# Kernel optimization log

Measured on AMD Instinct MI355X. Metric: run time of the kernel, lower is better.

## Reference

```python
import jax, jax.numpy as jnp
import numpy as np

NEG = -1e30  # finite stand-in for -inf so softmax grads stay clean


def setup_inputs() -> dict:
    key = jax.random.key(0)
    k1, k2 = jax.random.split(key)
    C, D = 8192, 512
    gt_class_embeddings = jax.random.normal(k1, (C, D), dtype=jnp.float32)
    w = jax.random.normal(k2, (C, D), dtype=jnp.float32)
    return {"gt_class_embeddings": gt_class_embeddings, "w": w}


def reference(gt_class_embeddings, w):
    # L2-normalize class embeddings, cosine-similarity matrix S (diag == 1)
    G = gt_class_embeddings / jnp.linalg.norm(gt_class_embeddings, axis=-1, keepdims=True)
    S = G @ G.T  # [C, C]
    C = S.shape[0]
    off_diag = ~jnp.eye(C, dtype=bool)

    # seSoftmax: per-row softmax over entries != 1 (off-diagonal); diagonal stays 1
    P = jax.nn.softmax(jnp.where(off_diag, S, NEG), axis=-1)
    S2 = jnp.where(off_diag, P, 1.0)

    # argsort(-S2)[1] == most similar (diag value 1 always ranks first),
    # argsort(-S2)[-1] == least similar == row min (softmax values < 1)
    ms = jnp.argmax(jnp.where(off_diag, S2, NEG), axis=-1)  # [C]
    ls = jnp.argmin(jnp.where(off_diag, S2, -NEG), axis=-1)  # [C]

    rows = jnp.arange(C)
    margin = S2[rows, ms] - S2[rows, ls]  # [C]

    d_ms = jnp.sqrt(jnp.sum((w - w[ms]) ** 2, axis=-1))  # [C]
    d_ls = jnp.sqrt(jnp.sum((w - w[ls]) ** 2, axis=-1))  # [C]

    loss = jnp.mean(jnp.maximum(0.0, d_ms - d_ls + margin))
    return loss
```

## Files before the change

### kernel.cpp

```cpp
#include <hip/hip_runtime.h>
#include <math.h>

#define CDIM 8192
#define DDIM 512
#define NEGF -3.0e38f
#define POSF  3.0e38f

#define BM 128
#define NSLOT (CDIM / BM)

typedef __attribute__((ext_vector_type(8))) short bf16x8;
typedef __attribute__((ext_vector_type(4))) float f32x4;

__device__ __forceinline__ unsigned short f2bf(float x) {
    unsigned int u = __float_as_uint(x);
    u += 0x7fffu + ((u >> 16) & 1u);
    return (unsigned short)(u >> 16);
}
__device__ __forceinline__ float bf2f(unsigned short h) {
    return __uint_as_float(((unsigned int)h) << 16);
}
__device__ __forceinline__ void gld16(const void* g, void* l) {
    __builtin_amdgcn_global_load_lds(
        (__attribute__((address_space(1))) void*)(void*)g,
        (__attribute__((address_space(3))) void*)l, 16, 0, 0);
}

__global__ __launch_bounds__(256) void k_prep(const float* __restrict__ g,
                                              unsigned short* __restrict__ hi,
                                              unsigned short* __restrict__ lo) {
    const int wave = threadIdx.x >> 6;
    const int lane = threadIdx.x & 63;
    const int row = blockIdx.x * 4 + wave;
    const float4* src = (const float4*)(g + (size_t)row * DDIM);
    const float4 a = src[lane * 2];
    const float4 b = src[lane * 2 + 1];
    float s = a.x * a.x + a.y * a.y + a.z * a.z + a.w * a.w +
              b.x * b.x + b.y * b.y + b.z * b.z + b.w * b.w;
#pragma unroll
    for (int m = 1; m < 64; m <<= 1) s += __shfl_xor(s, m, 64);
    const float rn = rsqrtf(s);
    const float y[8] = {a.x * rn, a.y * rn, a.z * rn, a.w * rn,
                        b.x * rn, b.y * rn, b.z * rn, b.w * rn};
    unsigned int hv[4], lv[4];
#pragma unroll
    for (int i = 0; i < 4; ++i) {
        const unsigned short h0 = f2bf(y[2 * i]);
        const unsigned short h1 = f2bf(y[2 * i + 1]);
        const unsigned short l0 = f2bf(y[2 * i] - bf2f(h0));
        const unsigned short l1 = f2bf(y[2 * i + 1] - bf2f(h1));
        hv[i] = (unsigned int)h0 | ((unsigned int)h1 << 16);
        lv[i] = (unsigned int)l0 | ((unsigned int)l1 << 16);
    }
    uint4* dh = (uint4*)(hi + (size_t)row * DDIM + lane * 8);
    uint4* dl = (uint4*)(lo + (size_t)row * DDIM + lane * 8);
    *dh = make_uint4(hv[0], hv[1], hv[2], hv[3]);
    *dl = make_uint4(lv[0], lv[1], lv[2], lv[3]);
}

__global__ __launch_bounds__(256, 3) void k_simstats(
    const unsigned short* __restrict__ ghi, const unsigned short* __restrict__ glo,
    float* __restrict__ pmax, float* __restrict__ pmin, float* __restrict__ pZ,
    int* __restrict__ pamax, int* __restrict__ pamin) {
    __shared__ unsigned short SH[4 * BM * 32];
    unsigned short* Ahi = SH;
    unsigned short* Alo = SH + 4096;
    unsigned short* Bhi = SH + 8192;
    unsigned short* Blo = SH + 12288;
    const int t = threadIdx.x;
    const int wave = t >> 6;
    const int lane = t & 63;
    const int lanelo = lane & 15;
    const int quad = lane >> 4;
    const int wr = wave & 1;
    const int wc = wave >> 1;

    const int bid = blockIdx.x;
    const int xcd = bid & 7;
    const int off = bid >> 3;
    int I, J, ntiles;
    if (off < 4) {
        const int d = xcd * 4 + off;
        I = 2 * d; J = I; ntiles = 2;
    } else {
        const int e = xcd * 252 + (off - 4);
        int Jf = (int)((1.0f + sqrtf(1.0f + 8.0f * (float)e)) * 0.5f);
        while ((Jf * (Jf - 1)) / 2 > e) --Jf;
        while (((Jf + 1) * Jf) / 2 <= e) ++Jf;
        J = Jf; I = e - (Jf * (Jf - 1)) / 2;
        ntiles = 1;
    }

    const int srow = t >> 2;
    const int scolb = ((t & 3) ^ ((t >> 3) & 3)) << 4;
    char* lAh = (char*)Ahi + t * 16;
    char* lAl = (char*)Alo + t * 16;
    char* lBh = (char*)Bhi + t * 16;
    char* lBl = (char*)Blo + t * 16;

    const int fsl = (quad ^ ((lanelo >> 1) & 3)) << 3;
    const int aoff = (wr * 64 + lanelo) * 32 + fsl;
    const int boff = (wc * 64 + lanelo) * 32 + fsl;

    float* rm  = (float*)SH;
    float* rz  = rm + 256;
    float* rmn = rz + 256;
    int*   ra  = (int*)(rmn + 256);
    int*   ran = ra + 256;
    float* cm  = (float*)Bhi;
    float* cz  = cm + 256;
    float* cmn = cz + 256;
    int*   ca  = (int*)(cmn + 256);
    int*   can = ca + 256;

    for (int tl = 0; tl < ntiles; ++tl) {
        const int Ie = I + tl, Je = J + tl;
        const int i0 = Ie * BM;
        const int j0 = Je * BM;
        const bool isdiag = (Ie == Je);

        f32x4 acc[4][4];
#pragma unroll
        for (int rt = 0; rt < 4; ++rt)
#pragma unroll
            for (int ct = 0; ct < 4; ++ct)
                acc[rt][ct] = (f32x4){0.f, 0.f, 0.f, 0.f};

        const char* baseAh = (const char*)ghi + (size_t)(i0 + srow) * 1024 + scolb;
        const char* baseAl = (const char*)glo + (size_t)(i0 + srow) * 1024 + scolb;
        const char* baseBh = (const char*)ghi + (size_t)(j0 + srow) * 1024 + scolb;
        const char* baseBl = (const char*)glo + (size_t)(j0 + srow) * 1024 + scolb;

        for (int k0 = 0; k0 < DDIM; k0 += 32) {
            __syncthreads();
#pragma unroll
            for (int q = 0; q < 2; ++q) {
                const size_t roff = (size_t)q * 64 * 1024 + k0 * 2;
                gld16(baseAh + roff, lAh + q * 4096);
                gld16(baseAl + roff, lAl + q * 4096);
                gld16(baseBh + roff, lBh + q * 4096);
                gld16(baseBl + roff, lBl + q * 4096);
            }
            __syncthreads();
            bf16x8 ah[4], al[4];
#pragma unroll
            for (int rt = 0; rt < 4; ++rt) {
                ah[rt] = *(const bf16x8*)&Ahi[aoff + rt * 512];
                al[rt] = *(const bf16x8*)&Alo[aoff + rt * 512];
            }
#pragma unroll
            for (int ct = 0; ct < 4; ++ct) {
                const bf16x8 bh = *(const bf16x8*)&Bhi[boff + ct * 512];
                const bf16x8 bl = *(const bf16x8*)&Blo[boff + ct * 512];
#pragma unroll
                for (int rt = 0; rt < 4; ++rt) {
                    acc[rt][ct] = __builtin_amdgcn_mfma_f32_16x16x32_bf16(
                        ah[rt], bh, acc[rt][ct], 0, 0, 0);
                    acc[rt][ct] = __builtin_amdgcn_mfma_f32_16x16x32_bf16(
                        ah[rt], bl, acc[rt][ct], 0, 0, 0);
                    acc[rt][ct] = __builtin_amdgcn_mfma_f32_16x16x32_bf16(
                        al[rt], bh, acc[rt][ct], 0, 0, 0);
                }
            }
        }

        __syncthreads();

#pragma unroll
        for (int rt = 0; rt < 4; ++rt) {
#pragma unroll
            for (int r = 0; r < 4; ++r) {
                const int lrow = wr * 64 + rt * 16 + quad * 4 + r;
                const int gi = i0 + lrow;
                float tmax = NEGF; int targ = 0x7fffffff;
                float tmin = POSF; int targn = 0x7fffffff;
#pragma unroll
                for (int ct = 0; ct < 4; ++ct) {
                    const int gj = j0 + wc * 64 + ct * 16 + lanelo;
                    const float v = acc[rt][ct][r];
                    const bool dg = isdiag && (gj == gi);
                    const float vM = dg ? NEGF : v;
                    const float vm = dg ? POSF : v;
                    if (vM > tmax) { tmax = vM; targ = gj; }
                    if (vm < tmin) { tmin = vm; targn = gj; }
                }
#pragma unroll
                for (int msk = 1; msk < 16; msk <<= 1) {
                    const float v2 = __shfl_xor(tmax, msk, 64);
                    const int i2 = __shfl_xor(targ, msk, 64);
                    if (v2 > tmax || (v2 == tmax && i2 < targ)) { tmax = v2; targ = i2; }
                    const float v3 = __shfl_xor(tmin, msk, 64);
                    const int i3 = __shfl_xor(targn, msk, 64);
                    if (v3 < tmin || (v3 == tmin && i3 < targn)) { tmin = v3; targn = i3; }
                }
                if (lanelo == 0) {
                    const int o = wc * 128 + lrow;
                    rm[o] = tmax; rmn[o] = tmin;
                    ra[o] = targ; ran[o] = targn;
                }
            }
        }

        if (!isdiag) {
#pragma unroll
            for (int ct = 0; ct < 4; ++ct) {
                const int lcol = wc * 64 + ct * 16 + lanelo;
                float tmax = NEGF; int targ = 0x7fffffff;
                float tmin = POSF; int targn = 0x7fffffff;
#pragma unroll
                for (int rt = 0; rt < 4; ++rt)
#pragma unroll
                    for (int r = 0; r < 4; ++r) {
                        const int gi = i0 + wr * 64 + rt * 16 + quad * 4 + r;
                        const float v = acc[rt][ct][r];
                        if (v > tmax) { tmax = v; targ = gi; }
                        if (v < tmin) { tmin = v; targn = gi; }
                    }
#pragma unroll
                for (int msk = 16; msk < 64; msk <<= 1) {
                    const float m2 = __shfl_xor(tmax, msk, 64);
                    const int i2 = __shfl_xor(targ, msk, 64);
                    if (m2 > tmax || (m2 == tmax && i2 < targ)) { tmax = m2; targ = i2; }
                    const float mn2 = __shfl_xor(tmin, msk, 64);
                    const int in2 = __shfl_xor(targn, msk, 64);
                    if (mn2 < tmin || (mn2 == tmin && in2 < targn)) { tmin = mn2; targn = in2; }
                }
                if (quad == 0) {
                    const int o = wr * 128 + lcol;
                    cm[o] = tmax; cmn[o] = tmin;
                    ca[o] = targ; can[o] = targn;
                }
            }
        }

#pragma unroll
        for (int rt = 0; rt < 4; ++rt)
#pragma unroll
            for (int ct = 0; ct < 4; ++ct)
#pragma unroll
                for (int r = 0; r < 4; ++r) {
                    float e = __expf(acc[rt][ct][r] - 1.f);
                    if (isdiag) {
                        const int gi = i0 + wr * 64 + rt * 16 + quad * 4 + r;
                        const int gj = j0 + wc * 64 + ct * 16 + lanelo;
                        if (gi == gj) e = 0.f;
                    }
                    acc[rt][ct][r] = e;
                }

#pragma unroll
        for (int rt = 0; rt < 4; ++rt)
#pragma unroll
            for (int r = 0; r < 4; ++r) {
                float s = acc[rt][0][r] + acc[rt][1][r] +
                          acc[rt][2][r] + acc[rt][3][r];
#pragma unroll
                for (int msk = 1; msk < 16; msk <<= 1) s += __shfl_xor(s, msk, 64);
                if (lanelo == 0)
                    rz[wc * 128 + wr * 64 + rt * 16 + quad * 4 + r] = s;
            }

        if (!isdiag) {
#pragma unroll
            for (int ct = 0; ct < 4; ++ct) {
                float s = 0.f;
#pragma unroll
                for (int rt = 0; rt < 4; ++rt)
                    s += acc[rt][ct][0] + acc[rt][ct][1] +
                         acc[rt][ct][2] + acc[rt][ct][3];
#pragma unroll
                for (int msk = 16; msk < 64; msk <<= 1) s += __shfl_xor(s, msk, 64);
                if (quad == 0)
                    cz[wr * 128 + wc * 64 + ct * 16 + lanelo] = s;
            }
        }

        __syncthreads();

        if (t < BM) {
            const float m0 = rm[t], m1 = rm[128 + t];
            float vmax = m0; int imax = ra[t];
            if (m1 > vmax) { vmax = m1; imax = ra[128 + t]; }
            float vmin = rmn[t]; int imin = ran[t];
            if (rmn[128 + t] < vmin) { vmin = rmn[128 + t]; imin = ran[128 + t]; }
            const size_t o = (size_t)Je * CDIM + i0 + t;
            pmax[o] = vmax; pmin[o] = vmin; pZ[o] = rz[t] + rz[128 + t];
            pamax[o] = imax; pamin[o] = imin;
        } else if (!isdiag) {
            const int tt = t - BM;
            const float m0 = cm[tt], m1 = cm[128 + tt];
            float vmax = m0; int imax = ca[tt];
            if (m1 > vmax) { vmax = m1; imax = ca[128 + tt]; }
            float vmin = cmn[tt]; int imin = can[tt];
            if (cmn[128 + tt] < vmin) { vmin = cmn[128 + tt]; imin = can[128 + tt]; }
            const size_t o = (size_t)Ie * CDIM + j0 + tt;
            pmax[o] = vmax; pmin[o] = vmin; pZ[o] = cz[tt] + cz[128 + tt];
            pamax[o] = imax; pamin[o] = imin;
        }
    }
}

__global__ __launch_bounds__(256) void k_lossc(
    const float* __restrict__ pmax, const float* __restrict__ pmin,
    const float* __restrict__ pZ, const int* __restrict__ pamax,
    const int* __restrict__ pamin, const float* __restrict__ w,
    float* __restrict__ vals) {
    const int wave = threadIdx.x >> 6;
    const int lane = threadIdx.x & 63;
    const int row = blockIdx.x * 4 + wave;
    const size_t o = (size_t)lane * CDIM + row;
    float v = pmax[o]; int a = pamax[o];
    float u = pmin[o]; int b = pamin[o];
    float z = pZ[o];
#pragma unroll
    for (int msk = 1; msk < 64; msk <<= 1) {
        const float v2 = __shfl_xor(v, msk, 64);
        const int i2 = __shfl_xor(a, msk, 64);
        if (v2 > v || (v2 == v && i2 < a)) { v = v2; a = i2; }
        const float v3 = __shfl_xor(u, msk, 64);
        const int i3 = __shfl_xor(b, msk, 64);
        if (v3 < u || (v3 == u && i3 < b)) { u = v3; b = i3; }
        z += __shfl_xor(z, msk, 64);
    }
    const float margin = (1.f - __expf(u - v)) * __expf(v - 1.f) / z;
    const int jm = a, jl = b;

    const float4* wi = (const float4*)(w + (size_t)row * DDIM);
    const float4* wm = (const float4*)(w + (size_t)jm * DDIM);
    const float4* wl = (const float4*)(w + (size_t)jl * DDIM);
    float sm = 0.f, sl = 0.f;
#pragma unroll
    for (int h = 0; h < 2; ++h) {
        const int idx = h * 64 + lane;
        const float4 x = wi[idx];
        const float4 y = wm[idx];
        const float4 c = wl[idx];
        float d;
        d = x.x - y.x; sm = fmaf(d, d, sm);
        d = x.y - y.y; sm = fmaf(d, d, sm);
        d = x.z - y.z; sm = fmaf(d, d, sm);
        d = x.w - y.w; sm = fmaf(d, d, sm);
        d = x.x - c.x; sl = fmaf(d, d, sl);
        d = x.y - c.y; sl = fmaf(d, d, sl);
        d = x.z - c.z; sl = fmaf(d, d, sl);
        d = x.w - c.w; sl = fmaf(d, d, sl);
    }
#pragma unroll
    for (int msk = 1; msk < 64; msk <<= 1) {
        sm += __shfl_xor(sm, msk, 64);
        sl += __shfl_xor(sl, msk, 64);
    }
    if (lane == 0) {
        const float val = sqrtf(sm) - sqrtf(sl) + margin;
        vals[row] = val > 0.f ? val : 0.f;
    }
}

__global__ __launch_bounds__(256) void k_final(const float* __restrict__ vals,
                                               float* __restrict__ out) {
    __shared__ float red[256];
    float s = 0.f;
    for (int i = threadIdx.x; i < CDIM; i += 256) s += vals[i];
    red[threadIdx.x] = s;
    __syncthreads();
#pragma unroll
    for (int k = 128; k > 0; k >>= 1) {
        if (threadIdx.x < (unsigned)k) red[threadIdx.x] += red[threadIdx.x + k];
        __syncthreads();
    }
    if (threadIdx.x == 0) out[0] = red[0] * (1.0f / CDIM);
}

extern "C" void kernel_launch(void* const* d_in, const int* in_sizes, int n_in,
                              void* d_out, int out_size, void* d_ws, size_t ws_size,
                              hipStream_t stream) {
    const float* g = (const float*)d_in[0];
    const float* w = (const float*)d_in[1];
    float* out = (float*)d_out;

    unsigned short* ghi = (unsigned short*)d_ws;
    unsigned short* glo = ghi + (size_t)CDIM * DDIM;
    float* p = (float*)(glo + (size_t)CDIM * DDIM);
    float* pmax = p;      p += (size_t)NSLOT * CDIM;
    float* pmin = p;      p += (size_t)NSLOT * CDIM;
    float* pZ = p;        p += (size_t)NSLOT * CDIM;
    int* pamax = (int*)p; p += (size_t)NSLOT * CDIM;
    int* pamin = (int*)p; p += (size_t)NSLOT * CDIM;
    float* vals = p;      p += CDIM;

    k_prep<<<CDIM / 4, 256, 0, stream>>>(g, ghi, glo);
    k_simstats<<<2048, 256, 0, stream>>>(ghi, glo, pmax, pmin, pZ, pamax, pamin);
    k_lossc<<<CDIM / 4, 256, 0, stream>>>(pmax, pmin, pZ, pamax, pamin, w, vals);
    k_final<<<1, 256, 0, stream>>>(vals, out);
}
```

Measured before the change: 253.9 us.

## Split partial-stat merge into coalesced kernel, specialize diag paths, drop tie-break compares

Replaces the wave-per-row merge of the 64 partial slots, which read strided columns, with a separate k_merge kernel in which each thread walks the slots for one row with coalesced loads. A second kernel, k_dist, then does the distance computation from stored margin and index arrays. The simstats epilogue gets a separate non-diagonal branch without diagonal masking, and applies the diagonal zeroing only to the tiles where wr==wc. Index tie-breaking in the shuffle reductions is dropped to save compares. The cost is one more launch, fewer blocks in the merge stage, and argmax/argmin on exact ties that may no longer pick the smallest index.

```diff
diff --git a/kernel.cpp b/kernel.cpp
--- a/kernel.cpp
+++ b/kernel.cpp
@@ -171,27 +171,37 @@
 #pragma unroll
             for (int r = 0; r < 4; ++r) {
                 const int lrow = wr * 64 + rt * 16 + quad * 4 + r;
-                const int gi = i0 + lrow;
-                float tmax = NEGF; int targ = 0x7fffffff;
-                float tmin = POSF; int targn = 0x7fffffff;
-#pragma unroll
-                for (int ct = 0; ct < 4; ++ct) {
-                    const int gj = j0 + wc * 64 + ct * 16 + lanelo;
-                    const float v = acc[rt][ct][r];
-                    const bool dg = isdiag && (gj == gi);
-                    const float vM = dg ? NEGF : v;
-                    const float vm = dg ? POSF : v;
-                    if (vM > tmax) { tmax = vM; targ = gj; }
-                    if (vm < tmin) { tmin = vm; targn = gj; }
+                float tmax = NEGF; int targ = 0;
+                float tmin = POSF; int targn = 0;
+                if (isdiag) {
+                    const int gi = i0 + lrow;
+#pragma unroll
+                    for (int ct = 0; ct < 4; ++ct) {
+                        const int gj = j0 + wc * 64 + ct * 16 + lanelo;
+                        const float v = acc[rt][ct][r];
+                        const bool dg = (gj == gi);
+                        const float vM = dg ? NEGF : v;
+                        const float vm = dg ? POSF : v;
+                        if (vM > tmax) { tmax = vM; targ = gj; }
+                        if (vm < tmin) { tmin = vm; targn = gj; }
+                    }
+                } else {
+#pragma unroll
+                    for (int ct = 0; ct < 4; ++ct) {
+                        const int gj = j0 + wc * 64 + ct * 16 + lanelo;
+                        const float v = acc[rt][ct][r];
+                        if (v > tmax) { tmax = v; targ = gj; }
+                        if (v < tmin) { tmin = v; targn = gj; }
+                    }
                 }
 #pragma unroll
                 for (int msk = 1; msk < 16; msk <<= 1) {
                     const float v2 = __shfl_xor(tmax, msk, 64);
                     const int i2 = __shfl_xor(targ, msk, 64);
-                    if (v2 > tmax || (v2 == tmax && i2 < targ)) { tmax = v2; targ = i2; }
+                    if (v2 > tmax) { tmax = v2; targ = i2; }
                     const float v3 = __shfl_xor(tmin, msk, 64);
                     const int i3 = __shfl_xor(targn, msk, 64);
-                    if (v3 < tmin || (v3 == tmin && i3 < targn)) { tmin = v3; targn = i3; }
+                    if (v3 < tmin) { tmin = v3; targn = i3; }
                 }
                 if (lanelo == 0) {
                     const int o = wc * 128 + lrow;
@@ -205,8 +215,8 @@
 #pragma unroll
             for (int ct = 0; ct < 4; ++ct) {
                 const int lcol = wc * 64 + ct * 16 + lanelo;
-                float tmax = NEGF; int targ = 0x7fffffff;
-                float tmin = POSF; int targn = 0x7fffffff;
+                float tmax = NEGF; int targ = 0;
+                float tmin = POSF; int targn = 0;
 #pragma unroll
                 for (int rt = 0; rt < 4; ++rt)
 #pragma unroll
@@ -220,10 +230,10 @@
                 for (int msk = 16; msk < 64; msk <<= 1) {
                     const float m2 = __shfl_xor(tmax, msk, 64);
                     const int i2 = __shfl_xor(targ, msk, 64);
-                    if (m2 > tmax || (m2 == tmax && i2 < targ)) { tmax = m2; targ = i2; }
+                    if (m2 > tmax) { tmax = m2; targ = i2; }
                     const float mn2 = __shfl_xor(tmin, msk, 64);
                     const int in2 = __shfl_xor(targn, msk, 64);
-                    if (mn2 < tmin || (mn2 == tmin && in2 < targn)) { tmin = mn2; targn = in2; }
+                    if (mn2 < tmin) { tmin = mn2; targn = in2; }
                 }
                 if (quad == 0) {
                     const int o = wr * 128 + lcol;
@@ -238,15 +248,15 @@
 #pragma unroll
             for (int ct = 0; ct < 4; ++ct)
 #pragma unroll
-                for (int r = 0; r < 4; ++r) {
-                    float e = __expf(acc[rt][ct][r] - 1.f);
-                    if (isdiag) {
-                        const int gi = i0 + wr * 64 + rt * 16 + quad * 4 + r;
-                        const int gj = j0 + wc * 64 + ct * 16 + lanelo;
-                        if (gi == gj) e = 0.f;
-                    }
-                    acc[rt][ct][r] = e;
-                }
+                for (int r = 0; r < 4; ++r)
+                    acc[rt][ct][r] = __expf(acc[rt][ct][r] - 1.f);
+        if (isdiag && wr == wc) {
+#pragma unroll
+            for (int rt = 0; rt < 4; ++rt)
+#pragma unroll
+                for (int r = 0; r < 4; ++r)
+                    if (lanelo == quad * 4 + r) acc[rt][rt][r] = 0.f;
+        }
 
 #pragma unroll
         for (int rt = 0; rt < 4; ++rt)
@@ -300,31 +310,38 @@
     }
 }
 
-__global__ __launch_bounds__(256) void k_lossc(
+__global__ __launch_bounds__(256) void k_merge(
     const float* __restrict__ pmax, const float* __restrict__ pmin,
     const float* __restrict__ pZ, const int* __restrict__ pamax,
-    const int* __restrict__ pamin, const float* __restrict__ w,
+    const int* __restrict__ pamin, float* __restrict__ margin,
+    int* __restrict__ ms, int* __restrict__ ls) {
+    const int row = blockIdx.x * 256 + threadIdx.x;
+    float M = NEGF; int a = 0;
+    float mn = POSF; int b = 0;
+    float Z = 0.f;
+    for (int s = 0; s < NSLOT; ++s) {
+        const size_t o = (size_t)s * CDIM + row;
+        const float v = pmax[o];
+        const int ia = pamax[o];
+        const float u = pmin[o];
+        const int ib = pamin[o];
+        Z += pZ[o];
+        if (v > M) { M = v; a = ia; }
+        if (u < mn) { mn = u; b = ib; }
+    }
+    margin[row] = (1.f - __expf(mn - M)) * __expf(M - 1.f) / Z;
+    ms[row] = a;
+    ls[row] = b;
+}
+
+__global__ __launch_bounds__(256) void k_dist(
+    const float* __restrict__ w, const float* __restrict__ margin,
+    const int* __restrict__ ms, const int* __restrict__ ls,
     float* __restrict__ vals) {
     const int wave = threadIdx.x >> 6;
     const int lane = threadIdx.x & 63;
     const int row = blockIdx.x * 4 + wave;
-    const size_t o = (size_t)lane * CDIM + row;
-    float v = pmax[o]; int a = pamax[o];
-    float u = pmin[o]; int b = pamin[o];
-    float z = pZ[o];
-#pragma unroll
-    for (int msk = 1; msk < 64; msk <<= 1) {
-        const float v2 = __shfl_xor(v, msk, 64);
-        const int i2 = __shfl_xor(a, msk, 64);
-        if (v2 > v || (v2 == v && i2 < a)) { v = v2; a = i2; }
-        const float v3 = __shfl_xor(u, msk, 64);
-        const int i3 = __shfl_xor(b, msk, 64);
-        if (v3 < u || (v3 == u && i3 < b)) { u = v3; b = i3; }
-        z += __shfl_xor(z, msk, 64);
-    }
-    const float margin = (1.f - __expf(u - v)) * __expf(v - 1.f) / z;
-    const int jm = a, jl = b;
-
+    const int jm = ms[row], jl = ls[row];
     const float4* wi = (const float4*)(w + (size_t)row * DDIM);
     const float4* wm = (const float4*)(w + (size_t)jm * DDIM);
     const float4* wl = (const float4*)(w + (size_t)jl * DDIM);
@@ -351,7 +368,7 @@
         sl += __shfl_xor(sl, msk, 64);
     }
     if (lane == 0) {
-        const float val = sqrtf(sm) - sqrtf(sl) + margin;
+        const float val = sqrtf(sm) - sqrtf(sl) + margin[row];
         vals[row] = val > 0.f ? val : 0.f;
     }
 }
@@ -387,9 +404,14 @@
     int* pamax = (int*)p; p += (size_t)NSLOT * CDIM;
     int* pamin = (int*)p; p += (size_t)NSLOT * CDIM;
     float* vals = p;      p += CDIM;
+    float* margin = p;    p += CDIM;
+    int* ms = (int*)p;    p += CDIM;
+    int* ls = (int*)p;    p += CDIM;
 
     k_prep<<<CDIM / 4, 256, 0, stream>>>(g, ghi, glo);
     k_simstats<<<2048, 256, 0, stream>>>(ghi, glo, pmax, pmin, pZ, pamax, pamin);
-    k_lossc<<<CDIM / 4, 256, 0, stream>>>(pmax, pmin, pZ, pamax, pamin, w, vals);
+    k_merge<<<CDIM / 256, 256, 0, stream>>>(pmax, pmin, pZ, pamax, pamin,
+                                            margin, ms, ls);
+    k_dist<<<CDIM / 4, 256, 0, stream>>>(w, margin, ms, ls, vals);
     k_final<<<1, 256, 0, stream>>>(vals, out);
 }
```

Result: no change. 249.8 us (-1.6%).
